# Kernel optimization log

Measured on AMD Instinct MI355X. Metric: run time of the kernel, lower is better.

## Reference

```python
import jax, jax.numpy as jnp
import numpy as np

E, H, I = 5, 768, 1024  # num_experts, hidden_dim, intermediate_dim
TOP_K = 2


def setup_inputs() -> dict:
    key = jax.random.key(0)
    ks = jax.random.split(key, 6)
    s = 0.02
    return {
        "x": jax.random.normal(ks[0], (4, 2048, H), dtype=jnp.float32),
        "router_w": jax.random.normal(ks[1], (E, H), dtype=jnp.float32) * s,  # torch Linear (out,in)
        "router_b": jnp.zeros((E,), dtype=jnp.float32),
        "gate_w": jax.random.normal(ks[2], (E, H, I), dtype=jnp.float32) * s,
        "up_w": jax.random.normal(ks[3], (E, H, I), dtype=jnp.float32) * s,
        "down_w": jax.random.normal(ks[4], (E, I, H), dtype=jnp.float32) * s,
    }


def reference(x, router_w, router_b, gate_w, up_w, down_w):
    B, S, Hd = x.shape
    xf = x.reshape(-1, Hd)                       # [T, H]
    T = xf.shape[0]
    # Router: linear (with bias) -> softmax -> top-2 -> renormalize
    logits = xf @ router_w.T + router_b          # [T, E]
    scores = jax.nn.softmax(logits, axis=-1)
    vals, idx = jax.lax.top_k(scores, TOP_K)     # [T, 2]
    vals = vals / jnp.sum(vals, axis=-1, keepdims=True)
    # Dense combine weights: zero for unselected experts (same math as the
    # per-expert gather/scatter loop in the original module).
    comb = jnp.zeros((T, gate_w.shape[0]), dtype=x.dtype)
    comb = comb.at[jnp.arange(T)[:, None], idx].add(vals)  # [T, E]
    # SwiGLU per expert, vectorized over experts
    g = jnp.einsum('th,ehi->tei', xf, gate_w)    # [T, E, I]
    u = jnp.einsum('th,ehi->tei', xf, up_w)
    y = jnp.einsum('tei,eih->teh', jax.nn.silu(g) * u, down_w)  # [T, E, H]
    out = jnp.einsum('teh,te->th', y, comb)
    return out.reshape(B, S, Hd)
```

## Files before the change

### kernel.cpp

```cpp
#include <hip/hip_runtime.h>
#include <hip/hip_bf16.h>
#include <cstdint>
#include <cstddef>

#define T_TOK 8192
#define H_DIM 768
#define I_DIM 1024
#define N_EXP 5

typedef short v8s __attribute__((ext_vector_type(8)));
typedef float v4f __attribute__((ext_vector_type(4)));

static __device__ __forceinline__ unsigned short f2bf(float f) {
    union { float f; unsigned int u; } v; v.f = f;
    unsigned int u = v.u;
    unsigned int r = (u + 0x7fffu + ((u >> 16) & 1u)) >> 16;
    return (unsigned short)r;
}

static __device__ __forceinline__ void async16(const unsigned short* g, unsigned short* l) {
    __builtin_amdgcn_global_load_lds(
        (const __attribute__((address_space(1))) unsigned int*)g,
        (__attribute__((address_space(3))) unsigned int*)l, 16, 0, 0);
}

__global__ void k_transp(const float* __restrict__ a, const float* __restrict__ b,
                         unsigned short* __restrict__ at, unsigned short* __restrict__ bt,
                         int R, int C) {
    __shared__ float tile[32][33];
    int z = blockIdx.z;
    int e = z % N_EXP;
    const float* src = (z < N_EXP ? a : b) + (size_t)e * R * C;
    unsigned short* dst = (z < N_EXP ? at : bt) + (size_t)e * R * C;
    int c0 = blockIdx.x * 32, r0 = blockIdx.y * 32;
    int tx = threadIdx.x, ty = threadIdx.y;
#pragma unroll
    for (int i = 0; i < 4; i++)
        tile[ty * 4 + i][tx] = src[(size_t)(r0 + ty * 4 + i) * C + c0 + tx];
    __syncthreads();
#pragma unroll
    for (int i = 0; i < 4; i++)
        dst[(size_t)(c0 + ty * 4 + i) * R + r0 + tx] = f2bf(tile[tx][ty * 4 + i]);
}

__global__ void k_router_a(const float* __restrict__ x, const float* __restrict__ rw,
                           const float* __restrict__ rb,
                           unsigned short* __restrict__ xb,
                           int* __restrict__ top2e, float2* __restrict__ top2w) {
    const int wave = threadIdx.x >> 6, lane = threadIdx.x & 63;
    const int t = blockIdx.x * 4 + wave;
    const float* xr = x + (size_t)t * H_DIM;
    unsigned short* xbr = xb + (size_t)t * H_DIM;
    float acc[N_EXP];
#pragma unroll
    for (int e = 0; e < N_EXP; e++) acc[e] = 0.f;
#pragma unroll
    for (int j = 0; j < H_DIM / 256; j++) {
        int idx = j * 256 + lane * 4;
        float4 xv = *(const float4*)(xr + idx);
        ushort4 o;
        o.x = f2bf(xv.x); o.y = f2bf(xv.y); o.z = f2bf(xv.z); o.w = f2bf(xv.w);
        *(ushort4*)(xbr + idx) = o;
#pragma unroll
        for (int e = 0; e < N_EXP; e++) {
            float4 wv = *(const float4*)(rw + e * H_DIM + idx);
            acc[e] += xv.x * wv.x + xv.y * wv.y + xv.z * wv.z + xv.w * wv.w;
        }
    }
#pragma unroll
    for (int s = 32; s > 0; s >>= 1) {
#pragma unroll
        for (int e = 0; e < N_EXP; e++) acc[e] += __shfl_down(acc[e], s);
    }
    if (lane == 0) {
        float l[N_EXP];
#pragma unroll
        for (int e = 0; e < N_EXP; e++) l[e] = acc[e] + rb[e];
        int i1 = 0;
#pragma unroll
        for (int e = 1; e < N_EXP; e++) if (l[e] > l[i1]) i1 = e;
        int i2 = (i1 == 0) ? 1 : 0;
#pragma unroll
        for (int e = 0; e < N_EXP; e++) if (e != i1 && l[e] > l[i2]) i2 = e;
        float w1 = 1.f / (1.f + __expf(l[i2] - l[i1]));
        top2e[t] = i1 | (i2 << 8);
        top2w[t] = make_float2(w1, 1.f - w1);
    }
}

__global__ void k_router_b(const int* __restrict__ top2e, const float2* __restrict__ top2w,
                           int* __restrict__ cnt, int* __restrict__ tokslot,
                           float* __restrict__ pweight) {
    __shared__ int lcnt[N_EXP], lbase[N_EXP];
    const int tid = threadIdx.x;
    if (tid < N_EXP) lcnt[tid] = 0;
    __syncthreads();
    const int t = blockIdx.x * 256 + tid;
    const int pe = top2e[t];
    const float2 wv = top2w[t];
    const int e1 = pe & 0xff, e2 = pe >> 8;
    const int s1 = atomicAdd(&lcnt[e1], 1);
    const int s2 = atomicAdd(&lcnt[e2], 1);
    __syncthreads();
    if (tid < N_EXP) lbase[tid] = atomicAdd(&cnt[tid], lcnt[tid]);
    __syncthreads();
    const int p1 = lbase[e1] + s1;
    tokslot[e1 * T_TOK + p1] = t; pweight[e1 * T_TOK + p1] = wv.x;
    const int p2 = lbase[e2] + s2;
    tokslot[e2 * T_TOK + p2] = t; pweight[e2 * T_TOK + p2] = wv.y;
}

__launch_bounds__(256, 2)
__global__ void k_gateup(const unsigned short* __restrict__ xb,
                         const unsigned short* __restrict__ gbt,
                         const unsigned short* __restrict__ ubt,
                         const int* __restrict__ cnt,
                         const int* __restrict__ tokslot,
                         const float* __restrict__ pweight,
                         unsigned short* __restrict__ hbuf) {
    const int e = blockIdx.z;
    const int cn = cnt[e];
    const int m0 = blockIdx.x * 128;
    if (m0 >= cn) return;
    int off = 0;
    for (int i = 0; i < e; i++) off += cnt[i];
    const int n0 = blockIdx.y * 64;

    __shared__ __align__(16) unsigned short ldsA[128 * 32];
    __shared__ __align__(16) unsigned short ldsB[128 * 32];
    __shared__ int tokLds[128];
    __shared__ float pwLds[128];

    const int tid = threadIdx.x;
    if (tid < 128) {
        int gr = m0 + tid;
        int tk = 0; float pw = 0.f;
        if (gr < cn) { tk = tokslot[e * T_TOK + gr]; pw = pweight[e * T_TOK + gr]; }
        tokLds[tid] = tk; pwLds[tid] = pw;
    }
    __syncthreads();

    const int lane = tid & 63;
    const int wave = tid >> 6;
    const int fm = lane & 15, quad = lane >> 4;

    const int srow = wave * 16 + (lane >> 2);
    const int scol = (lane & 3) * 8;
    const unsigned short* aG1 = xb + (size_t)tokLds[srow] * H_DIM + scol;
    const unsigned short* aG2 = xb + (size_t)tokLds[64 + srow] * H_DIM + scol;
    const unsigned short* bG1 = gbt + ((size_t)e * I_DIM + n0 + srow) * H_DIM + scol;
    const unsigned short* bG2 = ubt + ((size_t)e * I_DIM + n0 + srow) * H_DIM + scol;
    unsigned short* lA1 = ldsA + wave * 512;
    unsigned short* lA2 = ldsA + 2048 + wave * 512;
    unsigned short* lB1 = ldsB + wave * 512;
    unsigned short* lB2 = ldsB + 2048 + wave * 512;

    const int wm = wave * 32;

    v4f acc[2][8];
#pragma unroll
    for (int i = 0; i < 2; i++)
#pragma unroll
        for (int j = 0; j < 8; j++) acc[i][j] = (v4f)0.f;

    for (int kb = 0; kb < H_DIM / 32; kb++) {
        const int k0 = kb * 32;
        async16(aG1 + k0, lA1);
        async16(aG2 + k0, lA2);
        async16(bG1 + k0, lB1);
        async16(bG2 + k0, lB2);
        __syncthreads();
        v8s aF[2], bF[8];
#pragma unroll
        for (int im = 0; im < 2; im++)
            aF[im] = *(const v8s*)&ldsA[(wm + im * 16 + fm) * 32 + quad * 8];
#pragma unroll
        for (int in = 0; in < 8; in++)
            bF[in] = *(const v8s*)&ldsB[(in * 16 + fm) * 32 + quad * 8];
#pragma unroll
        for (int im = 0; im < 2; im++)
#pragma unroll
            for (int in = 0; in < 8; in++)
                acc[im][in] = __builtin_amdgcn_mfma_f32_16x16x32_bf16(aF[im], bF[in], acc[im][in], 0, 0, 0);
        __syncthreads();
    }

#pragma unroll
    for (int im = 0; im < 2; im++) {
#pragma unroll
        for (int reg = 0; reg < 4; reg++) {
            int lr = wm + im * 16 + quad * 4 + reg;
            int gr = m0 + lr;
            if (gr < cn) {
                float pw = pwLds[lr];
                size_t base = (size_t)(off + gr) * I_DIM + n0 + fm;
#pragma unroll
                for (int in = 0; in < 4; in++) {
                    float g = acc[im][in][reg];
                    float u = acc[im][in + 4][reg];
                    float s = g / (1.f + __expf(-g));
                    hbuf[base + in * 16] = f2bf(s * u * pw);
                }
            }
        }
    }
}

__launch_bounds__(256, 2)
__global__ void k_down(const unsigned short* __restrict__ hbuf,
                       const unsigned short* __restrict__ dbt,
                       const int* __restrict__ cnt,
                       const int* __restrict__ tokslot,
                       float* __restrict__ out) {
    const int e = blockIdx.z;
    const int cn = cnt[e];
    const int m0 = blockIdx.x * 128;
    if (m0 >= cn) return;
    int off = 0;
    for (int i = 0; i < e; i++) off += cnt[i];
    const int n0 = blockIdx.y * 128;

    __shared__ __align__(16) unsigned short ldsA[128 * 32];
    __shared__ __align__(16) unsigned short ldsB[128 * 32];
    __shared__ int tokLds[128];

    const int tid = threadIdx.x;
    if (tid < 128) {
        int gr = m0 + tid;
        tokLds[tid] = (gr < cn) ? tokslot[e * T_TOK + gr] : 0;
    }
    __syncthreads();

    const int lane = tid & 63;
    const int wave = tid >> 6;
    const int fm = lane & 15, quad = lane >> 4;

    const int srow = wave * 16 + (lane >> 2);
    const int scol = (lane & 3) * 8;
    int ar1 = m0 + srow;      if (ar1 >= cn) ar1 = cn - 1;
    int ar2 = m0 + 64 + srow; if (ar2 >= cn) ar2 = cn - 1;
    const unsigned short* aG1 = hbuf + (size_t)(off + ar1) * I_DIM + scol;
    const unsigned short* aG2 = hbuf + (size_t)(off + ar2) * I_DIM + scol;
    const unsigned short* bG1 = dbt + ((size_t)e * H_DIM + n0 + srow) * I_DIM + scol;
    const unsigned short* bG2 = dbt + ((size_t)e * H_DIM + n0 + 64 + srow) * I_DIM + scol;
    unsigned short* lA1 = ldsA + wave * 512;
    unsigned short* lA2 = ldsA + 2048 + wave * 512;
    unsigned short* lB1 = ldsB + wave * 512;
    unsigned short* lB2 = ldsB + 2048 + wave * 512;

    const int wm = (wave & 1) * 64, wn = (wave >> 1) * 64;

    v4f acc[4][4];
#pragma unroll
    for (int i = 0; i < 4; i++)
#pragma unroll
        for (int j = 0; j < 4; j++) acc[i][j] = (v4f)0.f;

    for (int kb = 0; kb < I_DIM / 32; kb++) {
        const int k0 = kb * 32;
        async16(aG1 + k0, lA1);
        async16(aG2 + k0, lA2);
        async16(bG1 + k0, lB1);
        async16(bG2 + k0, lB2);
        __syncthreads();
        v8s aF[4], bF[4];
#pragma unroll
        for (int im = 0; im < 4; im++)
            aF[im] = *(const v8s*)&ldsA[(wm + im * 16 + fm) * 32 + quad * 8];
#pragma unroll
        for (int in = 0; in < 4; in++)
            bF[in] = *(const v8s*)&ldsB[(wn + in * 16 + fm) * 32 + quad * 8];
#pragma unroll
        for (int im = 0; im < 4; im++)
#pragma unroll
            for (int in = 0; in < 4; in++)
                acc[im][in] = __builtin_amdgcn_mfma_f32_16x16x32_bf16(aF[im], bF[in], acc[im][in], 0, 0, 0);
        __syncthreads();
    }

#pragma unroll
    for (int im = 0; im < 4; im++) {
#pragma unroll
        for (int reg = 0; reg < 4; reg++) {
            int lr = wm + im * 16 + quad * 4 + reg;
            int gr = m0 + lr;
            if (gr < cn) {
                int tok = tokLds[lr];
#pragma unroll
                for (int in = 0; in < 4; in++) {
                    int col = n0 + wn + in * 16 + fm;
                    atomicAdd(&out[(size_t)tok * H_DIM + col], acc[im][in][reg]);
                }
            }
        }
    }
}

extern "C" void kernel_launch(void* const* d_in, const int* in_sizes, int n_in,
                              void* d_out, int out_size, void* d_ws, size_t ws_size,
                              hipStream_t stream) {
    const float* x  = (const float*)d_in[0];
    const float* rw = (const float*)d_in[1];
    const float* rb = (const float*)d_in[2];
    const float* gw = (const float*)d_in[3];
    const float* uw = (const float*)d_in[4];
    const float* dw = (const float*)d_in[5];
    float* out = (float*)d_out;

    char* ws = (char*)d_ws;
    size_t o = 0;
    auto alloc = [&](size_t bytes) { void* p = ws + o; o += (bytes + 255) & ~255ull; return p; };
    int*   cnt     = (int*)  alloc(N_EXP * 4);
    int*   tokslot = (int*)  alloc((size_t)N_EXP * T_TOK * 4);
    float* pweight = (float*)alloc((size_t)N_EXP * T_TOK * 4);
    int*   top2e   = (int*)  alloc((size_t)T_TOK * 4);
    float2* top2w  = (float2*)alloc((size_t)T_TOK * 8);
    unsigned short* xb   = (unsigned short*)alloc((size_t)T_TOK * H_DIM * 2);
    unsigned short* gbt  = (unsigned short*)alloc((size_t)N_EXP * H_DIM * I_DIM * 2);
    unsigned short* ubt  = (unsigned short*)alloc((size_t)N_EXP * H_DIM * I_DIM * 2);
    unsigned short* dbt  = (unsigned short*)alloc((size_t)N_EXP * H_DIM * I_DIM * 2);
    unsigned short* hbuf = (unsigned short*)alloc((size_t)2 * T_TOK * I_DIM * 2);

    hipMemsetAsync(cnt, 0, N_EXP * 4, stream);
    hipMemsetAsync(d_out, 0, (size_t)out_size * 4, stream);

    dim3 tg1(I_DIM / 32, H_DIM / 32, 2 * N_EXP);
    k_transp<<<tg1, dim3(32, 8), 0, stream>>>(gw, uw, gbt, ubt, H_DIM, I_DIM);
    dim3 tg2(H_DIM / 32, I_DIM / 32, N_EXP);
    k_transp<<<tg2, dim3(32, 8), 0, stream>>>(dw, dw, dbt, dbt, I_DIM, H_DIM);

    k_router_a<<<T_TOK / 4, 256, 0, stream>>>(x, rw, rb, xb, top2e, top2w);
    k_router_b<<<T_TOK / 256, 256, 0, stream>>>(top2e, top2w, cnt, tokslot, pweight);

    dim3 g1(T_TOK / 128, I_DIM / 64, N_EXP);
    k_gateup<<<g1, 256, 0, stream>>>(xb, gbt, ubt, cnt, tokslot, pweight, hbuf);

    dim3 g2(T_TOK / 128, H_DIM / 128, N_EXP);
    k_down<<<g2, 256, 0, stream>>>(hbuf, dbt, cnt, tokslot, out);
}
```

Before: 286.1 us.

## Compact expert tile scheduling, interleave gate/up weights, replace atomics with combine pass

Adds a tile-list kernel so the GEMM grids launch only the needed 128-row tiles instead of a full per-expert grid where most blocks exit early. Interleaves the gate and up weights in 16-row groups so each wave computes a 64x64 tile with a 4x4 MFMA layout and pairs gate/up accumulators locally. The down projection now writes bf16 partial outputs into per-slot buffers, and a separate combine kernel sums them, removing float atomics and the output memset. The cost is an extra kernel launch, extra buffer traffic, and bf16 rounding of the partial outputs.

After: 265.9 us. 1.08x faster.

```diff
diff --git a/kernel.cpp b/kernel.cpp
--- a/kernel.cpp
+++ b/kernel.cpp
@@ -7,6 +7,7 @@
 #define H_DIM 768
 #define I_DIM 1024
 #define N_EXP 5
+#define MAXTILE 136
 
 typedef short v8s __attribute__((ext_vector_type(8)));
 typedef float v4f __attribute__((ext_vector_type(4)));
@@ -17,6 +18,9 @@
     unsigned int r = (u + 0x7fffu + ((u >> 16) & 1u)) >> 16;
     return (unsigned short)r;
 }
+static __device__ __forceinline__ float bf2f(unsigned short s) {
+    union { unsigned int u; float f; } v; v.u = ((unsigned int)s) << 16; return v.f;
+}
 
 static __device__ __forceinline__ void async16(const unsigned short* g, unsigned short* l) {
     __builtin_amdgcn_global_load_lds(
@@ -24,23 +28,41 @@
         (__attribute__((address_space(3))) unsigned int*)l, 16, 0, 0);
 }
 
-__global__ void k_transp(const float* __restrict__ a, const float* __restrict__ b,
-                         unsigned short* __restrict__ at, unsigned short* __restrict__ bt,
-                         int R, int C) {
+__global__ void k_transp_wi(const float* __restrict__ gw, const float* __restrict__ uw,
+                            unsigned short* __restrict__ wbt) {
     __shared__ float tile[32][33];
     int z = blockIdx.z;
     int e = z % N_EXP;
-    const float* src = (z < N_EXP ? a : b) + (size_t)e * R * C;
-    unsigned short* dst = (z < N_EXP ? at : bt) + (size_t)e * R * C;
+    int isUp = z >= N_EXP;
+    const float* src = (isUp ? uw : gw) + (size_t)e * H_DIM * I_DIM;
     int c0 = blockIdx.x * 32, r0 = blockIdx.y * 32;
     int tx = threadIdx.x, ty = threadIdx.y;
 #pragma unroll
     for (int i = 0; i < 4; i++)
-        tile[ty * 4 + i][tx] = src[(size_t)(r0 + ty * 4 + i) * C + c0 + tx];
-    __syncthreads();
-#pragma unroll
-    for (int i = 0; i < 4; i++)
-        dst[(size_t)(c0 + ty * 4 + i) * R + r0 + tx] = f2bf(tile[tx][ty * 4 + i]);
+        tile[ty * 4 + i][tx] = src[(size_t)(r0 + ty * 4 + i) * I_DIM + c0 + tx];
+    __syncthreads();
+#pragma unroll
+    for (int i = 0; i < 4; i++) {
+        int c = c0 + ty * 4 + i;
+        int row = (c >> 4) * 32 + (c & 15) + (isUp ? 16 : 0);
+        wbt[((size_t)e * 2 * I_DIM + row) * H_DIM + r0 + tx] = f2bf(tile[tx][ty * 4 + i]);
+    }
+}
+
+__global__ void k_transp_d(const float* __restrict__ dw, unsigned short* __restrict__ dbt) {
+    __shared__ float tile[32][33];
+    int e = blockIdx.z;
+    const float* src = dw + (size_t)e * I_DIM * H_DIM;
+    unsigned short* dst = dbt + (size_t)e * I_DIM * H_DIM;
+    int c0 = blockIdx.x * 32, r0 = blockIdx.y * 32;
+    int tx = threadIdx.x, ty = threadIdx.y;
+#pragma unroll
+    for (int i = 0; i < 4; i++)
+        tile[ty * 4 + i][tx] = src[(size_t)(r0 + ty * 4 + i) * H_DIM + c0 + tx];
+    __syncthreads();
+#pragma unroll
+    for (int i = 0; i < 4; i++)
+        dst[(size_t)(c0 + ty * 4 + i) * I_DIM + r0 + tx] = f2bf(tile[tx][ty * 4 + i]);
 }
 
 __global__ void k_router_a(const float* __restrict__ x, const float* __restrict__ rw,
@@ -107,23 +129,35 @@
     const int p1 = lbase[e1] + s1;
     tokslot[e1 * T_TOK + p1] = t; pweight[e1 * T_TOK + p1] = wv.x;
     const int p2 = lbase[e2] + s2;
-    tokslot[e2 * T_TOK + p2] = t; pweight[e2 * T_TOK + p2] = wv.y;
+    tokslot[e2 * T_TOK + p2] = t | (1 << 16); pweight[e2 * T_TOK + p2] = wv.y;
+}
+
+__global__ void k_tiles(const int* __restrict__ cnt, int4* __restrict__ tiles) {
+    const int tid = threadIdx.x;
+    if (tid < MAXTILE) tiles[tid] = make_int4(-1, 0, 0, 0);
+    __syncthreads();
+    if (tid == 0) {
+        int off = 0, idx = 0;
+        for (int e = 0; e < N_EXP; e++) {
+            int cn = cnt[e];
+            for (int m0 = 0; m0 < cn; m0 += 128)
+                tiles[idx++] = make_int4(e, m0, off, cn);
+            off += cn;
+        }
+    }
 }
 
 __launch_bounds__(256, 2)
 __global__ void k_gateup(const unsigned short* __restrict__ xb,
-                         const unsigned short* __restrict__ gbt,
-                         const unsigned short* __restrict__ ubt,
-                         const int* __restrict__ cnt,
+                         const unsigned short* __restrict__ wbt,
+                         const int4* __restrict__ tiles,
                          const int* __restrict__ tokslot,
                          const float* __restrict__ pweight,
                          unsigned short* __restrict__ hbuf) {
-    const int e = blockIdx.z;
-    const int cn = cnt[e];
-    const int m0 = blockIdx.x * 128;
-    if (m0 >= cn) return;
-    int off = 0;
-    for (int i = 0; i < e; i++) off += cnt[i];
+    const int4 td = tiles[blockIdx.x];
+    const int e = td.x;
+    if (e < 0) return;
+    const int m0 = td.y, offe = td.z, cn = td.w;
     const int n0 = blockIdx.y * 64;
 
     __shared__ __align__(16) unsigned short ldsA[128 * 32];
@@ -135,7 +169,7 @@
     if (tid < 128) {
         int gr = m0 + tid;
         int tk = 0; float pw = 0.f;
-        if (gr < cn) { tk = tokslot[e * T_TOK + gr]; pw = pweight[e * T_TOK + gr]; }
+        if (gr < cn) { tk = tokslot[e * T_TOK + gr] & 0xFFFF; pw = pweight[e * T_TOK + gr]; }
         tokLds[tid] = tk; pwLds[tid] = pw;
     }
     __syncthreads();
@@ -148,20 +182,20 @@
     const int scol = (lane & 3) * 8;
     const unsigned short* aG1 = xb + (size_t)tokLds[srow] * H_DIM + scol;
     const unsigned short* aG2 = xb + (size_t)tokLds[64 + srow] * H_DIM + scol;
-    const unsigned short* bG1 = gbt + ((size_t)e * I_DIM + n0 + srow) * H_DIM + scol;
-    const unsigned short* bG2 = ubt + ((size_t)e * I_DIM + n0 + srow) * H_DIM + scol;
+    const unsigned short* bG1 = wbt + ((size_t)e * 2 * I_DIM + n0 * 2 + srow) * H_DIM + scol;
+    const unsigned short* bG2 = wbt + ((size_t)e * 2 * I_DIM + n0 * 2 + 64 + srow) * H_DIM + scol;
     unsigned short* lA1 = ldsA + wave * 512;
     unsigned short* lA2 = ldsA + 2048 + wave * 512;
     unsigned short* lB1 = ldsB + wave * 512;
     unsigned short* lB2 = ldsB + 2048 + wave * 512;
 
-    const int wm = wave * 32;
-
-    v4f acc[2][8];
-#pragma unroll
-    for (int i = 0; i < 2; i++)
-#pragma unroll
-        for (int j = 0; j < 8; j++) acc[i][j] = (v4f)0.f;
+    const int wm = (wave & 1) * 64, wnw = wave >> 1;
+
+    v4f acc[4][4];
+#pragma unroll
+    for (int i = 0; i < 4; i++)
+#pragma unroll
+        for (int j = 0; j < 4; j++) acc[i][j] = (v4f)0.f;
 
     for (int kb = 0; kb < H_DIM / 32; kb++) {
         const int k0 = kb * 32;
@@ -170,36 +204,36 @@
         async16(bG1 + k0, lB1);
         async16(bG2 + k0, lB2);
         __syncthreads();
-        v8s aF[2], bF[8];
-#pragma unroll
-        for (int im = 0; im < 2; im++)
+        v8s aF[4], bF[4];
+#pragma unroll
+        for (int im = 0; im < 4; im++)
             aF[im] = *(const v8s*)&ldsA[(wm + im * 16 + fm) * 32 + quad * 8];
 #pragma unroll
-        for (int in = 0; in < 8; in++)
-            bF[in] = *(const v8s*)&ldsB[(in * 16 + fm) * 32 + quad * 8];
-#pragma unroll
-        for (int im = 0; im < 2; im++)
-#pragma unroll
-            for (int in = 0; in < 8; in++)
+        for (int in = 0; in < 4; in++)
+            bF[in] = *(const v8s*)&ldsB[(wnw * 64 + in * 16 + fm) * 32 + quad * 8];
+#pragma unroll
+        for (int im = 0; im < 4; im++)
+#pragma unroll
+            for (int in = 0; in < 4; in++)
                 acc[im][in] = __builtin_amdgcn_mfma_f32_16x16x32_bf16(aF[im], bF[in], acc[im][in], 0, 0, 0);
         __syncthreads();
     }
 
 #pragma unroll
-    for (int im = 0; im < 2; im++) {
+    for (int im = 0; im < 4; im++) {
 #pragma unroll
         for (int reg = 0; reg < 4; reg++) {
             int lr = wm + im * 16 + quad * 4 + reg;
             int gr = m0 + lr;
             if (gr < cn) {
                 float pw = pwLds[lr];
-                size_t base = (size_t)(off + gr) * I_DIM + n0 + fm;
-#pragma unroll
-                for (int in = 0; in < 4; in++) {
-                    float g = acc[im][in][reg];
-                    float u = acc[im][in + 4][reg];
+                size_t base = (size_t)(offe + gr) * I_DIM + n0 + wnw * 32 + fm;
+#pragma unroll
+                for (int j = 0; j < 2; j++) {
+                    float g = acc[im][2 * j][reg];
+                    float u = acc[im][2 * j + 1][reg];
                     float s = g / (1.f + __expf(-g));
-                    hbuf[base + in * 16] = f2bf(s * u * pw);
+                    hbuf[base + j * 16] = f2bf(s * u * pw);
                 }
             }
         }
@@ -209,15 +243,13 @@
 __launch_bounds__(256, 2)
 __global__ void k_down(const unsigned short* __restrict__ hbuf,
                        const unsigned short* __restrict__ dbt,
-                       const int* __restrict__ cnt,
+                       const int4* __restrict__ tiles,
                        const int* __restrict__ tokslot,
-                       float* __restrict__ out) {
-    const int e = blockIdx.z;
-    const int cn = cnt[e];
-    const int m0 = blockIdx.x * 128;
-    if (m0 >= cn) return;
-    int off = 0;
-    for (int i = 0; i < e; i++) off += cnt[i];
+                       unsigned short* __restrict__ ybuf) {
+    const int4 td = tiles[blockIdx.x];
+    const int e = td.x;
+    if (e < 0) return;
+    const int m0 = td.y, offe = td.z, cn = td.w;
     const int n0 = blockIdx.y * 128;
 
     __shared__ __align__(16) unsigned short ldsA[128 * 32];
@@ -239,8 +271,8 @@
     const int scol = (lane & 3) * 8;
     int ar1 = m0 + srow;      if (ar1 >= cn) ar1 = cn - 1;
     int ar2 = m0 + 64 + srow; if (ar2 >= cn) ar2 = cn - 1;
-    const unsigned short* aG1 = hbuf + (size_t)(off + ar1) * I_DIM + scol;
-    const unsigned short* aG2 = hbuf + (size_t)(off + ar2) * I_DIM + scol;
+    const unsigned short* aG1 = hbuf + (size_t)(offe + ar1) * I_DIM + scol;
+    const unsigned short* aG2 = hbuf + (size_t)(offe + ar2) * I_DIM + scol;
     const unsigned short* bG1 = dbt + ((size_t)e * H_DIM + n0 + srow) * I_DIM + scol;
     const unsigned short* bG2 = dbt + ((size_t)e * H_DIM + n0 + 64 + srow) * I_DIM + scol;
     unsigned short* lA1 = ldsA + wave * 512;
@@ -285,15 +317,31 @@
             int lr = wm + im * 16 + quad * 4 + reg;
             int gr = m0 + lr;
             if (gr < cn) {
-                int tok = tokLds[lr];
+                int v = tokLds[lr];
+                int tok = v & 0xFFFF, s = (v >> 16) & 1;
 #pragma unroll
                 for (int in = 0; in < 4; in++) {
                     int col = n0 + wn + in * 16 + fm;
-                    atomicAdd(&out[(size_t)tok * H_DIM + col], acc[im][in][reg]);
+                    ybuf[((size_t)s * T_TOK + tok) * H_DIM + col] = f2bf(acc[im][in][reg]);
                 }
             }
         }
     }
+}
+
+__global__ void k_combine(const unsigned short* __restrict__ ybuf, float* __restrict__ out) {
+    const size_t i8 = ((size_t)blockIdx.x * 256 + threadIdx.x) * 8;
+    const unsigned short* y0 = ybuf + i8;
+    const unsigned short* y1 = ybuf + (size_t)T_TOK * H_DIM + i8;
+    ushort4 a0 = *(const ushort4*)y0, a1 = *(const ushort4*)(y0 + 4);
+    ushort4 b0 = *(const ushort4*)y1, b1 = *(const ushort4*)(y1 + 4);
+    float4 o0, o1;
+    o0.x = bf2f(a0.x) + bf2f(b0.x); o0.y = bf2f(a0.y) + bf2f(b0.y);
+    o0.z = bf2f(a0.z) + bf2f(b0.z); o0.w = bf2f(a0.w) + bf2f(b0.w);
+    o1.x = bf2f(a1.x) + bf2f(b1.x); o1.y = bf2f(a1.y) + bf2f(b1.y);
+    o1.z = bf2f(a1.z) + bf2f(b1.z); o1.w = bf2f(a1.w) + bf2f(b1.w);
+    *(float4*)(out + i8) = o0;
+    *(float4*)(out + i8 + 4) = o1;
 }
 
 extern "C" void kernel_launch(void* const* d_in, const int* in_sizes, int n_in,
@@ -315,26 +363,29 @@
     float* pweight = (float*)alloc((size_t)N_EXP * T_TOK * 4);
     int*   top2e   = (int*)  alloc((size_t)T_TOK * 4);
     float2* top2w  = (float2*)alloc((size_t)T_TOK * 8);
+    int4*  tiles   = (int4*) alloc((size_t)MAXTILE * 16);
     unsigned short* xb   = (unsigned short*)alloc((size_t)T_TOK * H_DIM * 2);
-    unsigned short* gbt  = (unsigned short*)alloc((size_t)N_EXP * H_DIM * I_DIM * 2);
-    unsigned short* ubt  = (unsigned short*)alloc((size_t)N_EXP * H_DIM * I_DIM * 2);
+    unsigned short* wbt  = (unsigned short*)alloc((size_t)N_EXP * 2 * I_DIM * H_DIM * 2);
     unsigned short* dbt  = (unsigned short*)alloc((size_t)N_EXP * H_DIM * I_DIM * 2);
     unsigned short* hbuf = (unsigned short*)alloc((size_t)2 * T_TOK * I_DIM * 2);
+    unsigned short* ybuf = (unsigned short*)alloc((size_t)2 * T_TOK * H_DIM * 2);
 
     hipMemsetAsync(cnt, 0, N_EXP * 4, stream);
-    hipMemsetAsync(d_out, 0, (size_t)out_size * 4, stream);
 
     dim3 tg1(I_DIM / 32, H_DIM / 32, 2 * N_EXP);
-    k_transp<<<tg1, dim3(32, 8), 0, stream>>>(gw, uw, gbt, ubt, H_DIM, I_DIM);
+    k_transp_wi<<<tg1, dim3(32, 8), 0, stream>>>(gw, uw, wbt);
     dim3 tg2(H_DIM / 32, I_DIM / 32, N_EXP);
-    k_transp<<<tg2, dim3(32, 8), 0, stream>>>(dw, dw, dbt, dbt, I_DIM, H_DIM);
+    k_transp_d<<<tg2, dim3(32, 8), 0, stream>>>(dw, dbt);
 
     k_router_a<<<T_TOK / 4, 256, 0, stream>>>(x, rw, rb, xb, top2e, top2w);
     k_router_b<<<T_TOK / 256, 256, 0, stream>>>(top2e, top2w, cnt, tokslot, pweight);
-
-    dim3 g1(T_TOK / 128, I_DIM / 64, N_EXP);
-    k_gateup<<<g1, 256, 0, stream>>>(xb, gbt, ubt, cnt, tokslot, pweight, hbuf);
-
-    dim3 g2(T_TOK / 128, H_DIM / 128, N_EXP);
-    k_down<<<g2, 256, 0, stream>>>(hbuf, dbt, cnt, tokslot, out);
-}
+    k_tiles<<<1, 256, 0, stream>>>(cnt, tiles);
+
+    dim3 g1(MAXTILE, I_DIM / 64);
+    k_gateup<<<g1, 256, 0, stream>>>(xb, wbt, tiles, tokslot, pweight, hbuf);
+
+    dim3 g2(MAXTILE, H_DIM / 128);
+    k_down<<<g2, 256, 0, stream>>>(hbuf, dbt, tiles, tokslot, ybuf);
+
+    k_combine<<<(T_TOK * H_DIM) / (256 * 8), 256, 0, stream>>>(ybuf, out);
+}
```
